# Performance work log

Hardware: AMD Instinct MI355X
Metric: run time of the kernel (lower is better)

## Reference

```python
import jax, jax.numpy as jnp
import numpy as np

N = 50000
E = 800000
IN_C = 128
OUT_C = 128
N_TYPES = 3
NEG_SLOPE = 0.2  # PyG GATConv default negative_slope


def setup_inputs() -> dict:
    key = jax.random.key(0)
    ks = jax.random.split(key, 10)
    x = jax.random.normal(ks[0], (N, IN_C), dtype=jnp.float32)
    edge_index = jax.random.randint(ks[1], (2, E), 0, N, dtype=jnp.int32)
    edge_type = jax.random.randint(ks[2], (E,), 0, N_TYPES, dtype=jnp.int32)
    node_type = jax.random.randint(ks[3], (N,), 0, 3, dtype=jnp.int32)
    s = 1.0 / np.sqrt(IN_C)
    emb_table = jax.random.normal(ks[4], (3, IN_C), dtype=jnp.float32)
    W = jax.random.normal(ks[5], (N_TYPES, IN_C, OUT_C), dtype=jnp.float32) * s
    att_src = jax.random.normal(ks[6], (N_TYPES, OUT_C), dtype=jnp.float32) * s
    att_dst = jax.random.normal(ks[7], (N_TYPES, OUT_C), dtype=jnp.float32) * s
    bias = jax.random.normal(ks[8], (N_TYPES, OUT_C), dtype=jnp.float32) * 0.01
    return {"x": x, "edge_index": edge_index, "edge_type": edge_type,
            "node_type": node_type, "emb_table": emb_table, "W": W,
            "att_src": att_src, "att_dst": att_dst, "bias": bias}


def reference(x, edge_index, edge_type, node_type, emb_table, W, att_src, att_dst, bias):
    # Eval mode: dropouts are identity. edge_index is non-empty -> GAT branch.
    n = x.shape[0]
    x = x + emb_table[node_type]  # node-type embedding add
    src, dst = edge_index[0], edge_index[1]
    out_sum = jnp.zeros((n, OUT_C), dtype=x.dtype)
    for t in range(N_TYPES):  # per-edge-type GATConv (heads=1, add_self_loops=True)
        xw = x @ W[t]                       # [N, out]
        a_s = xw @ att_src[t]               # [N] alpha_src per node
        a_d = xw @ att_dst[t]               # [N] alpha_dst per node
        mask = edge_type == t               # [E]
        e_raw = jax.nn.leaky_relu(a_s[src] + a_d[dst], NEG_SLOPE)  # [E]
        e_self = jax.nn.leaky_relu(a_s + a_d, NEG_SLOPE)           # [N] self-loop logit
        e_masked = jnp.where(mask, e_raw, -jnp.inf)
        m = jnp.maximum(jax.ops.segment_max(e_masked, dst, num_segments=n), e_self)
        m = jax.lax.stop_gradient(m)
        w_edge = jnp.where(mask, jnp.exp(e_raw - m[dst]), 0.0)     # [E]
        w_self = jnp.exp(e_self - m)                               # [N]
        denom = jax.ops.segment_sum(w_edge, dst, num_segments=n) + w_self
        num = jax.ops.segment_sum(w_edge[:, None] * xw[src], dst, num_segments=n) \
              + w_self[:, None] * xw
        out_sum = out_sum + num / denom[:, None] + bias[t]
        # (attention weights per type are w_edge/denom[dst]; only node output returned)
    return out_sum
```

## Files before the change

### kernel.cpp

```cpp
#include <hip/hip_runtime.h>
#include <math.h>

#define N_NODES 50000
#define N_EDGES 800000
#define C 128
#define NT 3
#define NEG 0.2f
#define CAP 64

#define GEMM_XB 782

typedef __attribute__((ext_vector_type(8))) short short8;
typedef __attribute__((ext_vector_type(4))) float f32x4;

__device__ __forceinline__ float leaky(float v) { return v > 0.f ? v : NEG * v; }

__device__ __forceinline__ unsigned short f2bf(float f) {
  unsigned int u = __float_as_uint(f);
  u = (u + 0x7FFFu + ((u >> 16) & 1u)) >> 16;
  return (unsigned short)u;
}
__device__ __forceinline__ float bf_lo(unsigned int w) { return __uint_as_float(w << 16); }
__device__ __forceinline__ float bf_hi(unsigned int w) { return __uint_as_float(w & 0xFFFF0000u); }

__global__ void k_prep(const float* __restrict__ W, unsigned short* __restrict__ Wt,
                       int* __restrict__ cnt) {
  int bid = blockIdx.x;
  if (bid < 192) {
    int idx = bid * 256 + threadIdx.x;
    int t = idx >> 14, rem = idx & 16383;
    int n = rem >> 7, k = rem & 127;
    Wt[((size_t)t * C + n) * C + k] = f2bf(W[((size_t)t * C + k) * C + n]);
  } else {
    int i4 = (bid - 192) * 256 + threadIdx.x;
    if (i4 < N_NODES / 4) ((int4*)cnt)[i4] = make_int4(0, 0, 0, 0);
  }
}

__global__ void k_main(const float* __restrict__ x, const int* __restrict__ node_type,
                       const float* __restrict__ emb, const unsigned short* __restrict__ Wt,
                       unsigned short* __restrict__ xwb,
                       const float* __restrict__ att_src, const float* __restrict__ att_dst,
                       float* __restrict__ a_s, float2* __restrict__ ad_es,
                       const int* __restrict__ ei, const int* __restrict__ etype,
                       int* __restrict__ cnt, int* __restrict__ buckets) {
  __shared__ unsigned short Bs[128][136];
  const int bid = blockIdx.x;
  const int tid = threadIdx.x;

  int gemm_id;
  if (bid < 2 * GEMM_XB) {
    if (bid & 1) {
      int e0 = ((bid >> 1) * 256 + tid) * 4;
      if (e0 + 4 <= N_EDGES) {
        int4 s4 = *(const int4*)(ei + e0);
        int4 d4 = *(const int4*)(ei + N_EDGES + e0);
        int4 t4 = *(const int4*)(etype + e0);
        int p0 = atomicAdd(&cnt[d4.x], 1);
        int p1 = atomicAdd(&cnt[d4.y], 1);
        int p2 = atomicAdd(&cnt[d4.z], 1);
        int p3 = atomicAdd(&cnt[d4.w], 1);
        if (p0 < CAP) buckets[(size_t)d4.x * CAP + p0] = t4.x * N_NODES + s4.x;
        if (p1 < CAP) buckets[(size_t)d4.y * CAP + p1] = t4.y * N_NODES + s4.y;
        if (p2 < CAP) buckets[(size_t)d4.z * CAP + p2] = t4.z * N_NODES + s4.z;
        if (p3 < CAP) buckets[(size_t)d4.w * CAP + p3] = t4.w * N_NODES + s4.w;
      }
      return;
    }
    gemm_id = bid >> 1;
  } else {
    gemm_id = bid - GEMM_XB;
  }
  const int t = gemm_id / GEMM_XB;
  const int rb = gemm_id - t * GEMM_XB;

  const int wid = tid >> 6, lane = tid & 63;
  const int m = lane & 15, quad = lane >> 4;
  const int row0 = rb * 64;
  const unsigned short* Wtt = Wt + (size_t)t * C * C;

  short8 af[4];
  {
    int arow = row0 + wid * 16 + m;
    bool valid = arow < N_NODES;
    const float* xr = x + (size_t)(valid ? arow : 0) * C;
    int nt = valid ? node_type[arow] : 0;
    const float* er = emb + nt * C;
#pragma unroll
    for (int k0i = 0; k0i < 4; ++k0i) {
      int cb = k0i * 32 + quad * 8;
      float4 v0 = *(const float4*)(xr + cb);
      float4 v1 = *(const float4*)(xr + cb + 4);
      float4 e0 = *(const float4*)(er + cb);
      float4 e1 = *(const float4*)(er + cb + 4);
      short8 f;
      f[0] = (short)f2bf(v0.x + e0.x);
      f[1] = (short)f2bf(v0.y + e0.y);
      f[2] = (short)f2bf(v0.z + e0.z);
      f[3] = (short)f2bf(v0.w + e0.w);
      f[4] = (short)f2bf(v1.x + e1.x);
      f[5] = (short)f2bf(v1.y + e1.y);
      f[6] = (short)f2bf(v1.z + e1.z);
      f[7] = (short)f2bf(v1.w + e1.w);
      af[k0i] = f;
    }
  }

#pragma unroll
  for (int it = 0; it < 8; ++it) {
    int c = tid + it * 256;
    int n = c >> 4, kc = c & 15;
    *(uint4*)&Bs[n][kc * 8] = *(const uint4*)(Wtt + (size_t)n * C + kc * 8);
  }
  __syncthreads();

  f32x4 acc[8] = {};
#pragma unroll
  for (int k0i = 0; k0i < 4; ++k0i) {
    int k0 = k0i * 32;
#pragma unroll
    for (int j = 0; j < 8; ++j) {
      short8 b = *(const short8*)&Bs[j * 16 + m][k0 + quad * 8];
      acc[j] = __builtin_amdgcn_mfma_f32_16x16x32_bf16(af[k0i], b, acc[j], 0, 0, 0);
    }
  }

  float ps[4] = {}, pd[4] = {};
#pragma unroll
  for (int j = 0; j < 8; ++j) {
    float as = att_src[t * C + j * 16 + m];
    float ad = att_dst[t * C + j * 16 + m];
#pragma unroll
    for (int reg = 0; reg < 4; ++reg) {
      int row = row0 + wid * 16 + quad * 4 + reg;
      float v = acc[j][reg];
      if (row < N_NODES) xwb[((size_t)t * N_NODES + row) * C + j * 16 + m] = f2bf(v);
      ps[reg] += v * as;
      pd[reg] += v * ad;
    }
  }
#pragma unroll
  for (int off = 1; off < 16; off <<= 1) {
#pragma unroll
    for (int reg = 0; reg < 4; ++reg) {
      ps[reg] += __shfl_xor(ps[reg], off);
      pd[reg] += __shfl_xor(pd[reg], off);
    }
  }
  if (m == 0) {
#pragma unroll
    for (int reg = 0; reg < 4; ++reg) {
      int row = row0 + wid * 16 + quad * 4 + reg;
      if (row < N_NODES) {
        int idx = t * N_NODES + row;
        a_s[idx] = ps[reg];
        ad_es[idx] = make_float2(pd[reg], leaky(ps[reg] + pd[reg]));
      }
    }
  }
}

__global__ void k_gather(const int* __restrict__ cnt, const int* __restrict__ buckets,
                         const unsigned short* __restrict__ xwb,
                         const float* __restrict__ a_s, const float2* __restrict__ ad_es,
                         const float* __restrict__ bias, float* __restrict__ out) {
  __shared__ float wcs[4][64];
  int wid = threadIdx.x >> 6;
  int lane = threadIdx.x & 63;
  int i = blockIdx.x * 4 + wid;
  int iu = __builtin_amdgcn_readfirstlane(i);
  const int* __restrict__ brow = buckets + (size_t)iu * CAP;
  int n = cnt[iu];
  if (n > CAP) n = CAP;

  int idxl = 0;
  if (lane < n) idxl = brow[lane];
  int tl = idxl >= 2 * N_NODES ? 2 : (idxl >= N_NODES ? 1 : 0);
  float as = a_s[idxl];
  float2 am = ad_es[tl * N_NODES + iu];
  float wl = (lane < n) ? __expf(leaky(as + am.x) - am.y) : 0.f;

  float s0 = tl == 0 ? wl : 0.f;
  float s1 = tl == 1 ? wl : 0.f;
  float s2 = tl == 2 ? wl : 0.f;
#pragma unroll
  for (int off = 1; off < 64; off <<= 1) {
    s0 += __shfl_xor(s0, off);
    s1 += __shfl_xor(s1, off);
    s2 += __shfl_xor(s2, off);
  }
  float inv3[NT] = {1.f / (s0 + 1.f), 1.f / (s1 + 1.f), 1.f / (s2 + 1.f)};
  wcs[wid][lane] = wl * inv3[tl];

  float acc0 = 0.f, acc1 = 0.f;
#pragma unroll
  for (int t = 0; t < NT; ++t) {
    int idx = t * N_NODES + iu;
    float coef = inv3[t];
    unsigned int w = ((const unsigned int*)(xwb + (size_t)idx * C))[lane];
    float2 b2 = ((const float2*)(bias + t * C))[lane];
    acc0 += coef * bf_lo(w) + b2.x;
    acc1 += coef * bf_hi(w) + b2.y;
  }

  const unsigned int* xwu = (const unsigned int*)xwb;
  int j = 0;
  for (; j + 16 <= n; j += 16) {
    float ac0 = 0.f, ac1 = 0.f;
#pragma unroll
    for (int k = 0; k < 16; ++k) {
      int idx = brow[j + k];
      float c = wcs[wid][j + k];
      unsigned int v = xwu[(size_t)idx * (C / 2) + lane];
      ac0 += c * bf_lo(v);
      ac1 += c * bf_hi(v);
    }
    acc0 += ac0; acc1 += ac1;
  }
  for (; j + 8 <= n; j += 8) {
    float ac0 = 0.f, ac1 = 0.f;
#pragma unroll
    for (int k = 0; k < 8; ++k) {
      int idx = brow[j + k];
      float c = wcs[wid][j + k];
      unsigned int v = xwu[(size_t)idx * (C / 2) + lane];
      ac0 += c * bf_lo(v);
      ac1 += c * bf_hi(v);
    }
    acc0 += ac0; acc1 += ac1;
  }
  for (; j < n; ++j) {
    int idx = brow[j];
    float c = wcs[wid][j];
    unsigned int v = xwu[(size_t)idx * (C / 2) + lane];
    acc0 += c * bf_lo(v);
    acc1 += c * bf_hi(v);
  }
  ((float2*)(out + (size_t)iu * C))[lane] = make_float2(acc0, acc1);
}

extern "C" void kernel_launch(void* const* d_in, const int* in_sizes, int n_in,
                              void* d_out, int out_size, void* d_ws, size_t ws_size,
                              hipStream_t stream) {
  const float* x       = (const float*)d_in[0];
  const int* edge_idx  = (const int*)d_in[1];
  const int* edge_type = (const int*)d_in[2];
  const int* node_type = (const int*)d_in[3];
  const float* emb     = (const float*)d_in[4];
  const float* W       = (const float*)d_in[5];
  const float* att_src = (const float*)d_in[6];
  const float* att_dst = (const float*)d_in[7];
  const float* bias    = (const float*)d_in[8];
  float* out = (float*)d_out;

  unsigned short* xwb = (unsigned short*)d_ws;
  unsigned short* Wt  = xwb + (size_t)NT * N_NODES * C;
  float*  a_s   = (float*)(Wt + (size_t)NT * C * C);
  float2* ad_es = (float2*)(a_s + (size_t)NT * N_NODES);
  int*    cnt   = (int*)(ad_es + (size_t)NT * N_NODES);
  int*    buckets = (int*)(cnt + N_NODES);

  k_prep<<<192 + 49, 256, 0, stream>>>(W, Wt, cnt);

  k_main<<<(NT + 1) * GEMM_XB, 256, 0, stream>>>(x, node_type, emb, Wt, xwb, att_src, att_dst,
                                                 a_s, ad_es, edge_idx, edge_type, cnt, buckets);

  k_gather<<<N_NODES / 4, 256, 0, stream>>>(cnt, buckets, xwb, a_s, ad_es, bias, out);
}
```

Measured before the change: 189.1 us.

## Loop all edge types per GEMM block and partition bucket atomics by destination range

Each GEMM block now loads its x row tile once and loops over all three edge-type weight matrices, reloading W into shared memory between types. This removes the extra 2*782 GEMM blocks that each re-read x and emb. The bucketing blocks are regrouped into four destination-range partitions. Every partition scans the whole edge list but only performs atomics for destinations inside its quarter, which is meant to improve atomic/L2 locality at the cost of reading the edge arrays four times. GEMM blocks become longer and serial across types, and the grid shrinks.

```diff
diff --git a/kernel.cpp b/kernel.cpp
--- a/kernel.cpp
+++ b/kernel.cpp
@@ -9,6 +9,7 @@
 #define CAP 64
 
 #define GEMM_XB 782
+#define NCHUNK 782
 
 typedef __attribute__((ext_vector_type(8))) short short8;
 typedef __attribute__((ext_vector_type(4))) float f32x4;
@@ -37,47 +38,54 @@
   }
 }
 
-__global__ void k_main(const float* __restrict__ x, const int* __restrict__ node_type,
-                       const float* __restrict__ emb, const unsigned short* __restrict__ Wt,
-                       unsigned short* __restrict__ xwb,
-                       const float* __restrict__ att_src, const float* __restrict__ att_dst,
-                       float* __restrict__ a_s, float2* __restrict__ ad_es,
-                       const int* __restrict__ ei, const int* __restrict__ etype,
-                       int* __restrict__ cnt, int* __restrict__ buckets) {
+__global__ void k_bm(const float* __restrict__ x, const int* __restrict__ node_type,
+                     const float* __restrict__ emb, const unsigned short* __restrict__ Wt,
+                     unsigned short* __restrict__ xwb,
+                     const float* __restrict__ att_src, const float* __restrict__ att_dst,
+                     float* __restrict__ a_s, float2* __restrict__ ad_es,
+                     const int* __restrict__ ei, const int* __restrict__ etype,
+                     int* __restrict__ cnt, int* __restrict__ buckets) {
   __shared__ unsigned short Bs[128][136];
   const int bid = blockIdx.x;
   const int tid = threadIdx.x;
 
-  int gemm_id;
-  if (bid < 2 * GEMM_XB) {
-    if (bid & 1) {
-      int e0 = ((bid >> 1) * 256 + tid) * 4;
+  if (bid & 1) {
+    const int j = bid >> 1;
+    const int c = j & 3;
+    const int i = j >> 2;
+    const int n_c = (c < 2) ? 196 : 195;
+    const int dlo = c * 12500, dhi = dlo + 12500;
+    for (int cc = i; cc < NCHUNK; cc += n_c) {
+      int e0 = cc * 1024 + tid * 4;
       if (e0 + 4 <= N_EDGES) {
         int4 s4 = *(const int4*)(ei + e0);
         int4 d4 = *(const int4*)(ei + N_EDGES + e0);
         int4 t4 = *(const int4*)(etype + e0);
-        int p0 = atomicAdd(&cnt[d4.x], 1);
-        int p1 = atomicAdd(&cnt[d4.y], 1);
-        int p2 = atomicAdd(&cnt[d4.z], 1);
-        int p3 = atomicAdd(&cnt[d4.w], 1);
-        if (p0 < CAP) buckets[(size_t)d4.x * CAP + p0] = t4.x * N_NODES + s4.x;
-        if (p1 < CAP) buckets[(size_t)d4.y * CAP + p1] = t4.y * N_NODES + s4.y;
-        if (p2 < CAP) buckets[(size_t)d4.z * CAP + p2] = t4.z * N_NODES + s4.z;
-        if (p3 < CAP) buckets[(size_t)d4.w * CAP + p3] = t4.w * N_NODES + s4.w;
-      }
-      return;
-    }
-    gemm_id = bid >> 1;
-  } else {
-    gemm_id = bid - GEMM_XB;
-  }
-  const int t = gemm_id / GEMM_XB;
-  const int rb = gemm_id - t * GEMM_XB;
-
+        if (d4.x >= dlo && d4.x < dhi) {
+          int p = atomicAdd(&cnt[d4.x], 1);
+          if (p < CAP) buckets[(size_t)d4.x * CAP + p] = t4.x * N_NODES + s4.x;
+        }
+        if (d4.y >= dlo && d4.y < dhi) {
+          int p = atomicAdd(&cnt[d4.y], 1);
+          if (p < CAP) buckets[(size_t)d4.y * CAP + p] = t4.y * N_NODES + s4.y;
+        }
+        if (d4.z >= dlo && d4.z < dhi) {
+          int p = atomicAdd(&cnt[d4.z], 1);
+          if (p < CAP) buckets[(size_t)d4.z * CAP + p] = t4.z * N_NODES + s4.z;
+        }
+        if (d4.w >= dlo && d4.w < dhi) {
+          int p = atomicAdd(&cnt[d4.w], 1);
+          if (p < CAP) buckets[(size_t)d4.w * CAP + p] = t4.w * N_NODES + s4.w;
+        }
+      }
+    }
+    return;
+  }
+
+  const int rb = bid >> 1;
   const int wid = tid >> 6, lane = tid & 63;
   const int m = lane & 15, quad = lane >> 4;
   const int row0 = rb * 64;
-  const unsigned short* Wtt = Wt + (size_t)t * C * C;
 
   short8 af[4];
   {
@@ -110,52 +118,66 @@
   for (int it = 0; it < 8; ++it) {
     int c = tid + it * 256;
     int n = c >> 4, kc = c & 15;
-    *(uint4*)&Bs[n][kc * 8] = *(const uint4*)(Wtt + (size_t)n * C + kc * 8);
+    *(uint4*)&Bs[n][kc * 8] = *(const uint4*)(Wt + (size_t)n * C + kc * 8);
   }
   __syncthreads();
 
-  f32x4 acc[8] = {};
-#pragma unroll
-  for (int k0i = 0; k0i < 4; ++k0i) {
-    int k0 = k0i * 32;
+  for (int t = 0; t < NT; ++t) {
+    f32x4 acc[8] = {};
+#pragma unroll
+    for (int k0i = 0; k0i < 4; ++k0i) {
+      int k0 = k0i * 32;
+#pragma unroll
+      for (int j = 0; j < 8; ++j) {
+        short8 b = *(const short8*)&Bs[j * 16 + m][k0 + quad * 8];
+        acc[j] = __builtin_amdgcn_mfma_f32_16x16x32_bf16(af[k0i], b, acc[j], 0, 0, 0);
+      }
+    }
+
+    float ps[4] = {}, pd[4] = {};
 #pragma unroll
     for (int j = 0; j < 8; ++j) {
-      short8 b = *(const short8*)&Bs[j * 16 + m][k0 + quad * 8];
-      acc[j] = __builtin_amdgcn_mfma_f32_16x16x32_bf16(af[k0i], b, acc[j], 0, 0, 0);
-    }
-  }
-
-  float ps[4] = {}, pd[4] = {};
-#pragma unroll
-  for (int j = 0; j < 8; ++j) {
-    float as = att_src[t * C + j * 16 + m];
-    float ad = att_dst[t * C + j * 16 + m];
-#pragma unroll
-    for (int reg = 0; reg < 4; ++reg) {
-      int row = row0 + wid * 16 + quad * 4 + reg;
-      float v = acc[j][reg];
-      if (row < N_NODES) xwb[((size_t)t * N_NODES + row) * C + j * 16 + m] = f2bf(v);
-      ps[reg] += v * as;
-      pd[reg] += v * ad;
-    }
-  }
-#pragma unroll
-  for (int off = 1; off < 16; off <<= 1) {
-#pragma unroll
-    for (int reg = 0; reg < 4; ++reg) {
-      ps[reg] += __shfl_xor(ps[reg], off);
-      pd[reg] += __shfl_xor(pd[reg], off);
-    }
-  }
-  if (m == 0) {
-#pragma unroll
-    for (int reg = 0; reg < 4; ++reg) {
-      int row = row0 + wid * 16 + quad * 4 + reg;
-      if (row < N_NODES) {
-        int idx = t * N_NODES + row;
-        a_s[idx] = ps[reg];
-        ad_es[idx] = make_float2(pd[reg], leaky(ps[reg] + pd[reg]));
-      }
+      float as = att_src[t * C + j * 16 + m];
+      float ad = att_dst[t * C + j * 16 + m];
+#pragma unroll
+      for (int reg = 0; reg < 4; ++reg) {
+        int row = row0 + wid * 16 + quad * 4 + reg;
+        float v = acc[j][reg];
+        if (row < N_NODES) xwb[((size_t)t * N_NODES + row) * C + j * 16 + m] = f2bf(v);
+        ps[reg] += v * as;
+        pd[reg] += v * ad;
+      }
+    }
+#pragma unroll
+    for (int off = 1; off < 16; off <<= 1) {
+#pragma unroll
+      for (int reg = 0; reg < 4; ++reg) {
+        ps[reg] += __shfl_xor(ps[reg], off);
+        pd[reg] += __shfl_xor(pd[reg], off);
+      }
+    }
+    if (m == 0) {
+#pragma unroll
+      for (int reg = 0; reg < 4; ++reg) {
+        int row = row0 + wid * 16 + quad * 4 + reg;
+        if (row < N_NODES) {
+          int idx = t * N_NODES + row;
+          a_s[idx] = ps[reg];
+          ad_es[idx] = make_float2(pd[reg], leaky(ps[reg] + pd[reg]));
+        }
+      }
+    }
+
+    if (t + 1 < NT) {
+      __syncthreads();
+      const unsigned short* Wtt = Wt + (size_t)(t + 1) * C * C;
+#pragma unroll
+      for (int it = 0; it < 8; ++it) {
+        int c = tid + it * 256;
+        int n = c >> 4, kc = c & 15;
+        *(uint4*)&Bs[n][kc * 8] = *(const uint4*)(Wtt + (size_t)n * C + kc * 8);
+      }
+      __syncthreads();
     }
   }
 }
@@ -262,8 +284,8 @@
 
   k_prep<<<192 + 49, 256, 0, stream>>>(W, Wt, cnt);
 
-  k_main<<<(NT + 1) * GEMM_XB, 256, 0, stream>>>(x, node_type, emb, Wt, xwb, att_src, att_dst,
-                                                 a_s, ad_es, edge_idx, edge_type, cnt, buckets);
+  k_bm<<<2 * GEMM_XB, 256, 0, stream>>>(x, node_type, emb, Wt, xwb, att_src, att_dst,
+                                        a_s, ad_es, edge_idx, edge_type, cnt, buckets);
 
   k_gather<<<N_NODES / 4, 256, 0, stream>>>(cnt, buckets, xwb, a_s, ad_es, bias, out);
 }
```

Result: faster. 176.8 us (median of 2 runs) (-6.5%).
